# Kernel optimization log

Hardware: AMD Instinct MI355X
Metric: run time of the kernel (lower is better)

## Reference

```python
import jax, jax.numpy as jnp
import numpy as np

EMBED_DIM = 256
NUM_HEADS = 8
MLP_HIDDEN = 1024
EPS = 1e-5
ROPE_BASE = 10000.0
NEG_INF = -1e9


def _ln(x, g, b):
    m = jnp.mean(x, axis=-1, keepdims=True)
    v = jnp.mean((x - m) ** 2, axis=-1, keepdims=True)
    return (x - m) / jnp.sqrt(v + EPS) * g + b


def _proj_qkv(x, W, b):
    # x: (B, L, E); W: (3E, E)
    qkv = x @ W.T + b
    q, k, v = jnp.split(qkv, 3, axis=-1)
    B, L, E = x.shape
    def h(t):
        return t.reshape(B, L, NUM_HEADS, E // NUM_HEADS).transpose(0, 2, 1, 3)
    return h(q), h(k), h(v)


def _rope(x, offset):
    # x: (B, H, L, hd), interleaved even/odd rotation
    hd = x.shape[-1]
    L = x.shape[-2]
    inv_freq = 1.0 / (ROPE_BASE ** (jnp.arange(0, hd, 2, dtype=jnp.float32) / hd))
    t = jnp.arange(L, dtype=jnp.float32) + offset
    freqs = t[:, None] * inv_freq[None, :]  # (L, hd/2)
    cos = jnp.cos(freqs)[None, None].astype(x.dtype)
    sin = jnp.sin(freqs)[None, None].astype(x.dtype)
    xe = x[..., 0::2]
    xo = x[..., 1::2]
    xr = jnp.stack((xe * cos - xo * sin, xe * sin + xo * cos), axis=-1)
    return xr.reshape(x.shape)


def _sdpa(q, k, v, bias):
    scale = 1.0 / jnp.sqrt(jnp.asarray(q.shape[-1], q.dtype))
    s = jnp.einsum('bhqd,bhkd->bhqk', q, k) * scale + bias
    p = jax.nn.softmax(s, axis=-1)
    return jnp.einsum('bhqk,bhkd->bhqd', p, v)


def _mha_self(x, in_w, in_b, out_w, out_b):
    q, k, v = _proj_qkv(x, in_w, in_b)
    o = _sdpa(q, k, v, jnp.zeros((), x.dtype))
    B, H, L, hd = o.shape
    o = o.transpose(0, 2, 1, 3).reshape(B, L, H * hd)
    return o @ out_w.T + out_b


def setup_inputs() -> dict:
    key = jax.random.key(0)
    ks = jax.random.split(key, 20)
    E, Hm = EMBED_DIM, MLP_HIDDEN
    sc = 0.02
    inp = {
        'src': jax.random.normal(ks[0], (8, 128, 64, E), dtype=jnp.float32),
        'src_mask': jax.random.randint(ks[1], (8, 128), 0, 2, dtype=jnp.int32),
        'ctx_qry_split_index': 96,
        'y_in_w': jax.random.normal(ks[2], (3 * E, E)) * sc,
        'y_in_b': jnp.zeros((3 * E,)),
        'y_out_w': jax.random.normal(ks[3], (E, E)) * sc,
        'y_out_b': jnp.zeros((E,)),
        'x_in_w': jax.random.normal(ks[4], (3 * E, E)) * sc,
        'x_in_b': jnp.zeros((3 * E,)),
        'x_out_w': jax.random.normal(ks[5], (E, E)) * sc,
        'x_out_b': jnp.zeros((E,)),
        'w1': jax.random.normal(ks[6], (Hm, E)) * sc,
        'b1': jnp.zeros((Hm,)),
        'w2': jax.random.normal(ks[7], (E, Hm)) * sc,
        'b2': jnp.zeros((E,)),
        'n1_g': jnp.ones((E,)), 'n1_b': jnp.zeros((E,)),
        'n2_g': jnp.ones((E,)), 'n2_b': jnp.zeros((E,)),
        'n3_g': jnp.ones((E,)), 'n3_b': jnp.zeros((E,)),
    }
    return inp


def reference(src, src_mask, ctx_qry_split_index,
              y_in_w, y_in_b, y_out_w, y_out_b,
              x_in_w, x_in_b, x_out_w, x_out_b,
              w1, b1, w2, b2,
              n1_g, n1_b, n2_g, n2_b, n3_g, n3_b):
    bs, R, C, E = src.shape
    S = int(ctx_qry_split_index)
    # ---- y (column-axis) self-attention ----
    x = src.reshape(bs * R, C, E)
    x = jnp.nan_to_num(x, nan=0.0, posinf=0.0, neginf=0.0)
    x = _mha_self(x, y_in_w, y_in_b, y_out_w, y_out_b) + x
    x = x.reshape(bs, R, C, E)
    x = _ln(x, n1_g, n1_b)
    # ---- x (row-axis) attention with ctx/qry split ----
    x = x.transpose(0, 2, 1, 3).reshape(bs * C, R, E)
    x = jnp.nan_to_num(x, nan=0.0, posinf=0.0, neginf=0.0)
    mask_x = jnp.broadcast_to((src_mask > 0)[:, None, :], (bs, C, R)).reshape(bs * C, R)
    kpm_ctx = ~mask_x[:, :S]  # (B, S) True = padded
    bias = jnp.where(kpm_ctx[:, None, None, :], jnp.asarray(NEG_INF, x.dtype), 0.0)
    src_ctx = x[:, :S, :]
    src_qry = x[:, S:, :]
    # ctx self-attention
    q_c, k_c, v_c = _proj_qkv(src_ctx, x_in_w, x_in_b)
    q_c = _rope(q_c, 0)
    k_c = _rope(k_c, 0)
    out_ctx = _sdpa(q_c, k_c, v_c, bias)
    B = bs * C
    out_ctx = out_ctx.transpose(0, 2, 1, 3).reshape(B, S, E)
    out_ctx = out_ctx @ x_out_w.T + x_out_b
    src_ctx = out_ctx + src_ctx
    # qry cross-attention into (updated) ctx
    q_q, _, _ = _proj_qkv(src_qry, x_in_w, x_in_b)
    _, k_c2, v_c2 = _proj_qkv(src_ctx, x_in_w, x_in_b)
    q_q = _rope(q_q, S)
    k_c2 = _rope(k_c2, 0)
    out_qry = _sdpa(q_q, k_c2, v_c2, bias)
    L_qry = R - S
    out_qry = out_qry.transpose(0, 2, 1, 3).reshape(B, L_qry, E)
    out_qry = out_qry @ x_out_w.T + x_out_b
    src_qry = out_qry + src_qry
    x = jnp.concatenate([src_ctx, src_qry], axis=1)
    x = x.reshape(bs, C, R, E).transpose(0, 2, 1, 3)
    x = _ln(x, n2_g, n2_b)
    # ---- FFN ----
    mlp = (jax.nn.gelu(x @ w1.T + b1, approximate=False)) @ w2.T + b2
    x = x + mlp
    return _ln(x, n3_g, n3_b)
```

## Files before the change

### kernel.cpp

```cpp
#include <hip/hip_runtime.h>
#include <hip/hip_bf16.h>
#include <math.h>


#define EDIM 256
#define HD   32
#define SCTX 96

typedef __bf16 bf16x8 __attribute__((ext_vector_type(8)));
typedef float  f32x4  __attribute__((ext_vector_type(4)));
union Frag { bf16x8 v; unsigned short u[8]; };

static __device__ __forceinline__ float b2f(unsigned short u) {
    return __uint_as_float(((unsigned int)u) << 16);
}
static __device__ __forceinline__ unsigned short f2b(float f) {
    unsigned int u = __float_as_uint(f);
    u += 0x7fffu + ((u >> 16) & 1u);
    return (unsigned short)(u >> 16);
}

static __device__ __forceinline__ void gload16(const unsigned short* g, unsigned short* l) {
    __builtin_amdgcn_global_load_lds(
        (const __attribute__((address_space(1))) unsigned int*)g,
        (__attribute__((address_space(3))) unsigned int*)l,
        16, 0, 0);
}

__global__ void detect_kernel(const unsigned int* __restrict__ n1g_raw,
                              int* __restrict__ flag) {
    *flag = (*n1g_raw == 0x3F800000u) ? 1 : 0;
}

struct PtrTable { const void* p[18]; };

__global__ void cvt_kernel(PtrTable t, const int* __restrict__ flag,
                           unsigned short* __restrict__ wp) {
    const int seg_off[19] = {0, 196608, 197376, 262912, 263168, 459776, 460544,
                             526080, 526336, 788480, 789504, 1051648, 1051904,
                             1052160, 1052416, 1052672, 1052928, 1053184, 1053440};
    const int f = *flag;
    int idx = blockIdx.x * blockDim.x + threadIdx.x;
    int stride = gridDim.x * blockDim.x;
    for (int i = idx; i < 1053440; i += stride) {
        int s = 0;
        while (i >= seg_off[s + 1]) ++s;
        int j = i - seg_off[s];
        unsigned short o;
        if (f) o = f2b(((const float*)t.p[s])[j]);
        else   o = ((const unsigned short*)t.p[s])[j];
        wp[i] = o;
    }
}

__global__ void prep_kernel(const void* __restrict__ src,
                            unsigned short* __restrict__ dst,
                            const int* __restrict__ flag, int n4) {
    const int f = *flag;
    int idx = blockIdx.x * blockDim.x + threadIdx.x;
    int stride = gridDim.x * blockDim.x;
    if (f) {
        const float4* s4 = (const float4*)src;
        for (int i = idx; i < n4; i += stride) {
            float4 v = s4[i];
            ushort4 o;
            o.x = ((__float_as_uint(v.x) & 0x7F800000u) == 0x7F800000u) ? 0 : f2b(v.x);
            o.y = ((__float_as_uint(v.y) & 0x7F800000u) == 0x7F800000u) ? 0 : f2b(v.y);
            o.z = ((__float_as_uint(v.z) & 0x7F800000u) == 0x7F800000u) ? 0 : f2b(v.z);
            o.w = ((__float_as_uint(v.w) & 0x7F800000u) == 0x7F800000u) ? 0 : f2b(v.w);
            ((ushort4*)dst)[i] = o;
        }
    } else {
        const ushort4* s4 = (const ushort4*)src;
        for (int i = idx; i < n4; i += stride) {
            ushort4 v = s4[i];
            if ((v.x & 0x7F80u) == 0x7F80u) v.x = 0;
            if ((v.y & 0x7F80u) == 0x7F80u) v.y = 0;
            if ((v.z & 0x7F80u) == 0x7F80u) v.z = 0;
            if ((v.w & 0x7F80u) == 0x7F80u) v.w = 0;
            ((ushort4*)dst)[i] = v;
        }
    }
}

__global__ __launch_bounds__(256) void gemm_mfma(
        const unsigned short* __restrict__ A, int lda,
        const unsigned short* __restrict__ W, int ldw,
        const unsigned short* __restrict__ bias,
        const unsigned short* __restrict__ res,
        unsigned short* __restrict__ out, int ldo,
        int K, int fuse, int pred, const int* __restrict__ splitp) {
    __shared__ __align__(16) unsigned short SH[16384];
    unsigned short* Asb  = SH;
    unsigned short* Bsb  = SH + 8192;
    unsigned short* Slab = SH;

    const int tid = threadIdx.x;

    const int nT   = gridDim.y;
    const int nwg  = gridDim.x * nT;
    const int flat = blockIdx.y * gridDim.x + blockIdx.x;
    const int cpx  = nwg >> 3;
    const int wgid = (flat & 7) * cpx + (flat >> 3);
    const int m0 = (wgid / nT) * 128;
    const int n0 = (wgid % nT) * 128;

    const int wave = tid >> 6;
    const int lane = tid & 63;
    const int wm = (wave >> 1) << 6;
    const int wn = (wave & 1) << 6;
    const int lm = lane & 15;
    const int lq = lane >> 4;

    const int rt = tid >> 3;
    const int ct = (tid & 7) * 8;
    const unsigned short* Ag = A + (size_t)(m0 + rt) * lda + ct;
    const unsigned short* Wg = W + (size_t)(n0 + rt) * ldw + ct;
    const size_t a32 = (size_t)32 * lda, w32 = (size_t)32 * ldw;
    unsigned short* Adst = Asb + wave * 512;
    unsigned short* Bdst = Bsb + wave * 512;

    f32x4 acc[4][4] = {};
    for (int k0 = 0; k0 < K; k0 += 64) {
        __syncthreads();
#pragma unroll
        for (int j = 0; j < 4; ++j) {
            gload16(Ag + j * a32 + k0, Adst + j * 2048);
            gload16(Wg + j * w32 + k0, Bdst + j * 2048);
        }
        __syncthreads();
#pragma unroll
        for (int kk = 0; kk < 2; ++kk) {
            const int ko = kk * 32 + lq * 8;
            bf16x8 af[4], bq[4];
#pragma unroll
            for (int i = 0; i < 4; ++i)
                af[i] = *(const bf16x8*)&Asb[(wm + i * 16 + lm) * 64 + ko];
#pragma unroll
            for (int j = 0; j < 4; ++j)
                bq[j] = *(const bf16x8*)&Bsb[(wn + j * 16 + lm) * 64 + ko];
#pragma unroll
            for (int i = 0; i < 4; ++i)
#pragma unroll
                for (int j = 0; j < 4; ++j)
                    acc[i][j] = __builtin_amdgcn_mfma_f32_16x16x32_bf16(af[i], bq[j], acc[i][j], 0, 0, 0);
        }
    }
    __syncthreads();

    const int S = (pred != 0) ? *splitp : 0;
    float bv[4];
#pragma unroll
    for (int j = 0; j < 4; ++j)
        bv[j] = bias ? b2f(bias[n0 + wn + j * 16 + lm]) : 0.f;

    const int srow = (wave >> 1) * 16 + lq * 4;
    const int sr2 = tid >> 3;
    const int cc = (tid & 7) * 16;
    const int mH = (sr2 >> 4) * 64 + (sr2 & 15);

#pragma unroll
    for (int i = 0; i < 4; ++i) {
#pragma unroll
        for (int j = 0; j < 4; ++j)
#pragma unroll
            for (int r = 0; r < 4; ++r) {
                float x = acc[i][j][r] + bv[j];
                if (fuse == 1) x = 0.5f * x * (1.0f + erff(x * 0.70710678118654752f));
                Slab[(srow + r) * 136 + wn + j * 16 + lm] = f2b(x);
            }
        __syncthreads();
        {
            const int m = m0 + mH + i * 16;
            const int rr = m & 127;
            bool st = true;
            if (pred == 1 && rr >= S) st = false;
            if (pred == 2 && rr < S) st = false;
            if (st) {
#pragma unroll
                for (int h = 0; h < 2; ++h) {
                    uint4 v = *(const uint4*)&Slab[sr2 * 136 + cc + h * 8];
                    if (res) {
                        uint4 rv = *(const uint4*)(res + (size_t)m * 256 + n0 + cc + h * 8);
                        unsigned short* pv = (unsigned short*)&v;
                        const unsigned short* pr = (const unsigned short*)&rv;
#pragma unroll
                        for (int e = 0; e < 8; ++e)
                            pv[e] = f2b(b2f(pv[e]) + b2f(pr[e]));
                    }
                    *(uint4*)(out + (size_t)m * ldo + n0 + cc + h * 8) = v;
                }
            }
        }
        __syncthreads();
    }
}

static __device__ __forceinline__ void rope8(float* t, int p0, float pos) {
#pragma unroll
    for (int p = 0; p < 4; ++p) {
        float invf = exp2f((float)(p0 + p) * -0.8304820237193385f);
        float ang = pos * invf;
        float c = __cosf(ang), s = __sinf(ang);
        float xe = t[2 * p], xo = t[2 * p + 1];
        t[2 * p]     = xe * c - xo * s;
        t[2 * p + 1] = xe * s + xo * c;
    }
}

template<int NQT, int NKT, bool ROPE, bool BIAS>
__global__ __launch_bounds__(64) void attn_mfma(unsigned short* __restrict__ QKV,
                                                const int* __restrict__ mask,
                                                int seqlen, int qoff) {
    constexpr int NK = NKT * 16;
    constexpr int KS = NK / 32;
    const int s = blockIdx.x;
    const int h = blockIdx.y;
    const int lane = threadIdx.x;
    const int lm = lane & 15;
    const int lq = lane >> 4;
    const size_t rowbase = (size_t)s * seqlen;
    const float scale = 0.17677669529663689f;

    __shared__ __align__(16) unsigned short Vs[NK][40];
    __shared__ __align__(16) unsigned short Pt[16][104];
    __shared__ float bias_s[NK];

#pragma unroll
    for (int r0 = 0; r0 < NK; r0 += 16) {
        int r = r0 + (lane >> 2);
        int c = (lane & 3) * 8;
        uint4 v = *(const uint4*)(QKV + (rowbase + r) * 768 + 512 + h * 32 + c);
        *(uint4*)&Vs[r][c] = v;
    }
    if (BIAS) {
        const int b = s >> 6;
        for (int r = lane; r < NK; r += 64)
            bias_s[r] = (mask[b * 128 + r] > 0) ? 0.f : -1e9f;
    }
    Frag kf[NKT];
#pragma unroll
    for (int nt = 0; nt < NKT; ++nt) {
        const int krow = nt * 16 + lm;
        const unsigned short* kp = QKV + (rowbase + krow) * 768 + 256 + h * 32 + lq * 8;
        float t[8];
#pragma unroll
        for (int j = 0; j < 8; ++j) t[j] = b2f(kp[j]);
        if (ROPE) rope8(t, lq * 4, (float)krow);
#pragma unroll
        for (int j = 0; j < 8; ++j) kf[nt].u[j] = f2b(t[j]);
    }
    __syncthreads();
    Frag bvf[KS][2];
#pragma unroll
    for (int ks = 0; ks < KS; ++ks)
#pragma unroll
        for (int dt = 0; dt < 2; ++dt)
#pragma unroll
            for (int j = 0; j < 8; ++j)
                bvf[ks][dt].u[j] = Vs[ks * 32 + lq * 8 + j][dt * 16 + lm];

    for (int mt = 0; mt < NQT; ++mt) {
        Frag qf;
        const int qrow = qoff + mt * 16 + lm;
        {
            const unsigned short* qp = QKV + (rowbase + qrow) * 768 + h * 32 + lq * 8;
            float t[8];
#pragma unroll
            for (int j = 0; j < 8; ++j) t[j] = b2f(qp[j]);
            if (ROPE) rope8(t, lq * 4, (float)qrow);
#pragma unroll
            for (int j = 0; j < 8; ++j) qf.u[j] = f2b(t[j]);
        }
        f32x4 sacc[NKT] = {};
#pragma unroll
        for (int nt = 0; nt < NKT; ++nt)
            sacc[nt] = __builtin_amdgcn_mfma_f32_16x16x32_bf16(qf.v, kf[nt].v, sacc[nt], 0, 0, 0);
        float pv[NKT][4], mx[4], sm[4], inv[4];
#pragma unroll
        for (int r = 0; r < 4; ++r) mx[r] = -3.0e38f;
#pragma unroll
        for (int nt = 0; nt < NKT; ++nt)
#pragma unroll
            for (int r = 0; r < 4; ++r) {
                float x = sacc[nt][r] * scale;
                if (BIAS) x += bias_s[nt * 16 + lm];
                pv[nt][r] = x;
                mx[r] = fmaxf(mx[r], x);
            }
#pragma unroll
        for (int m = 1; m < 16; m <<= 1)
#pragma unroll
            for (int r = 0; r < 4; ++r) mx[r] = fmaxf(mx[r], __shfl_xor(mx[r], m, 64));
#pragma unroll
        for (int r = 0; r < 4; ++r) sm[r] = 0.f;
#pragma unroll
        for (int nt = 0; nt < NKT; ++nt)
#pragma unroll
            for (int r = 0; r < 4; ++r) {
                float p = __expf(pv[nt][r] - mx[r]);
                pv[nt][r] = p;
                sm[r] += p;
            }
#pragma unroll
        for (int m = 1; m < 16; m <<= 1)
#pragma unroll
            for (int r = 0; r < 4; ++r) sm[r] += __shfl_xor(sm[r], m, 64);
#pragma unroll
        for (int r = 0; r < 4; ++r) inv[r] = 1.f / sm[r];
#pragma unroll
        for (int nt = 0; nt < NKT; ++nt)
#pragma unroll
            for (int r = 0; r < 4; ++r)
                Pt[lq * 4 + r][nt * 16 + lm] = f2b(pv[nt][r] * inv[r]);
        __syncthreads();
        f32x4 oacc[2] = {};
#pragma unroll
        for (int ks = 0; ks < KS; ++ks) {
            Frag af;
            af.v = *(const bf16x8*)&Pt[lm][ks * 32 + lq * 8];
#pragma unroll
            for (int dt = 0; dt < 2; ++dt)
                oacc[dt] = __builtin_amdgcn_mfma_f32_16x16x32_bf16(af.v, bvf[ks][dt].v, oacc[dt], 0, 0, 0);
        }
#pragma unroll
        for (int dt = 0; dt < 2; ++dt)
#pragma unroll
            for (int r = 0; r < 4; ++r) {
                const int m = qoff + mt * 16 + lq * 4 + r;
                QKV[(rowbase + m) * 768 + h * 32 + dt * 16 + lm] = f2b(oacc[dt][r]);
            }
        __syncthreads();
    }
}

__global__ __launch_bounds__(64) void ln_permute_kernel(
        const unsigned short* __restrict__ X,
        const unsigned short* __restrict__ gam,
        const unsigned short* __restrict__ bet,
        void* __restrict__ Y, int mode, const int* __restrict__ flag) {
    const int t = blockIdx.x;
    const int tid = threadIdx.x;
    const int e = tid << 2;
    ushort4 xv = *(const ushort4*)(X + (size_t)t * EDIM + e);
    float v0 = b2f(xv.x), v1 = b2f(xv.y), v2 = b2f(xv.z), v3 = b2f(xv.w);
    float s = v0 + v1 + v2 + v3;
#pragma unroll
    for (int m = 32; m > 0; m >>= 1) s += __shfl_xor(s, m, 64);
    float mean = s * (1.f / EDIM);
    float d0 = v0 - mean, d1 = v1 - mean, d2 = v2 - mean, d3 = v3 - mean;
    float q = d0 * d0 + d1 * d1 + d2 * d2 + d3 * d3;
#pragma unroll
    for (int m = 32; m > 0; m >>= 1) q += __shfl_xor(q, m, 64);
    float rstd = rsqrtf(q * (1.f / EDIM) + 1e-5f);
    float g0 = b2f(gam[e]), g1 = b2f(gam[e + 1]), g2 = b2f(gam[e + 2]), g3 = b2f(gam[e + 3]);
    float b0 = b2f(bet[e]), b1 = b2f(bet[e + 1]), b2_ = b2f(bet[e + 2]), b3 = b2f(bet[e + 3]);
    float y0 = d0 * rstd * g0 + b0;
    float y1 = d1 * rstd * g1 + b1;
    float y2 = d2 * rstd * g2 + b2_;
    float y3 = d3 * rstd * g3 + b3;
    size_t drow;
    if (mode == 0) {
        int b = t >> 13, r = (t >> 6) & 127, c = t & 63;
        drow = ((size_t)b << 13) + ((size_t)c << 7) + (size_t)r;
    } else if (mode == 1) {
        int b = t >> 13, c = (t >> 7) & 63, r = t & 127;
        drow = ((size_t)b << 13) + ((size_t)r << 6) + (size_t)c;
    } else {
        drow = (size_t)t;
    }
    if (mode == 2 && *flag) {
        float4 o4 = make_float4(y0, y1, y2, y3);
        *(float4*)((float*)Y + drow * EDIM + e) = o4;
    } else {
        ushort4 o;
        o.x = f2b(y0); o.y = f2b(y1); o.z = f2b(y2); o.w = f2b(y3);
        *(ushort4*)((unsigned short*)Y + drow * EDIM + e) = o;
    }
}

extern "C" void kernel_launch(void* const* d_in, const int* in_sizes, int n_in,
                              void* d_out, int out_size, void* d_ws, size_t ws_size,
                              hipStream_t stream) {
    (void)in_sizes; (void)n_in; (void)out_size; (void)ws_size;
    const void* src  = d_in[0];
    const int*  mask = (const int*)d_in[1];
    const int*  split= (const int*)d_in[2];

    int*            flag = (int*)d_ws;
    unsigned short* wp   = (unsigned short*)((char*)d_ws + 1024);
    unsigned short* Xa   = (unsigned short*)((char*)d_ws + (size_t)4 * 1024 * 1024);
    unsigned short* Xb   = Xa + (size_t)16777216;
    unsigned short* QKV  = Xb + (size_t)16777216;
    unsigned short* HID  = QKV;

    const unsigned short* y_in_w  = wp + 0;
    const unsigned short* y_in_b  = wp + 196608;
    const unsigned short* y_out_w = wp + 197376;
    const unsigned short* y_out_b = wp + 262912;
    const unsigned short* x_in_w  = wp + 263168;
    const unsigned short* x_in_b  = wp + 459776;
    const unsigned short* x_out_w = wp + 460544;
    const unsigned short* x_out_b = wp + 526080;
    const unsigned short* w1      = wp + 526336;
    const unsigned short* b1      = wp + 788480;
    const unsigned short* w2      = wp + 789504;
    const unsigned short* b2      = wp + 1051648;
    const unsigned short* n1_g    = wp + 1051904;
    const unsigned short* n1_b    = wp + 1052160;
    const unsigned short* n2_g    = wp + 1052416;
    const unsigned short* n2_b    = wp + 1052672;
    const unsigned short* n3_g    = wp + 1052928;
    const unsigned short* n3_b    = wp + 1053184;

    detect_kernel<<<1, 1, 0, stream>>>((const unsigned int*)d_in[15], flag);

    PtrTable pt;
    for (int i = 0; i < 18; ++i) pt.p[i] = d_in[3 + i];
    cvt_kernel<<<512, 256, 0, stream>>>(pt, flag, wp);

    prep_kernel<<<4096, 256, 0, stream>>>(src, Xa, flag, 4194304);
    gemm_mfma<<<dim3(512, 6), 256, 0, stream>>>(Xa, 256, y_in_w, 256, y_in_b, nullptr, QKV, 768, 256, 0, 0, nullptr);
    attn_mfma<4, 4, false, false><<<dim3(1024, 8), 64, 0, stream>>>(QKV, mask, 64, 0);
    gemm_mfma<<<dim3(512, 2), 256, 0, stream>>>(QKV, 768, y_out_w, 256, y_out_b, Xa, Xa, 256, 256, 0, 0, nullptr);
    ln_permute_kernel<<<65536, 64, 0, stream>>>(Xa, n1_g, n1_b, Xb, 0, flag);
    gemm_mfma<<<dim3(512, 6), 256, 0, stream>>>(Xb, 256, x_in_w, 256, x_in_b, nullptr, QKV, 768, 256, 0, 0, nullptr);
    attn_mfma<6, 6, true, true><<<dim3(512, 8), 64, 0, stream>>>(QKV, mask, 128, 0);
    gemm_mfma<<<dim3(512, 2), 256, 0, stream>>>(QKV, 768, x_out_w, 256, x_out_b, Xb, Xb, 256, 256, 0, 1, split);
    gemm_mfma<<<dim3(512, 4), 256, 0, stream>>>(Xb, 256, x_in_w + 65536, 256, x_in_b + 256, nullptr, QKV + 256, 768, 256, 0, 0, nullptr);
    attn_mfma<2, 6, true, true><<<dim3(512, 8), 64, 0, stream>>>(QKV, mask, 128, 96);
    gemm_mfma<<<dim3(512, 2), 256, 0, stream>>>(QKV, 768, x_out_w, 256, x_out_b, Xb, Xb, 256, 256, 0, 2, split);
    ln_permute_kernel<<<65536, 64, 0, stream>>>(Xb, n2_g, n2_b, Xa, 1, flag);
    gemm_mfma<<<dim3(512, 4), 256, 0, stream>>>(Xa, 256, w1, 256, b1, nullptr, HID, 512, 256, 1, 0, nullptr);
    gemm_mfma<<<dim3(512, 2), 256, 0, stream>>>(HID, 512, w2, 1024, b2, Xa, Xb, 256, 512, 0, 0, nullptr);
    gemm_mfma<<<dim3(512, 4), 256, 0, stream>>>(Xa, 256, w1 + 512 * 256, 256, b1 + 512, nullptr, HID, 512, 256, 1, 0, nullptr);
    gemm_mfma<<<dim3(512, 2), 256, 0, stream>>>(HID, 512, w2 + 512, 1024, nullptr, Xb, Xb, 256, 512, 0, 0, nullptr);
    ln_permute_kernel<<<65536, 64, 0, stream>>>(Xb, n3_g, n3_b, d_out, 2, flag);
}
```

Baseline: 746.3 us.

## Double-buffer GEMM LDS tiles to overlap global loads with MFMA

Doubles the shared-memory buffer in the MFMA GEMM kernel so the next K-tile is fetched into LDS via global_load_lds while the current tile is being multiplied. This also drops one barrier per K step. The aim is to hide global memory latency behind compute. In exchange, LDS use rises to 64KB per block, which may reduce occupancy. Correctness now relies on a single barrier per iteration covering both the async load completion and the buffer reuse.

```diff
diff --git a/kernel.cpp b/kernel.cpp
--- a/kernel.cpp
+++ b/kernel.cpp
@@ -90,9 +90,7 @@
         const unsigned short* __restrict__ res,
         unsigned short* __restrict__ out, int ldo,
         int K, int fuse, int pred, const int* __restrict__ splitp) {
-    __shared__ __align__(16) unsigned short SH[16384];
-    unsigned short* Asb  = SH;
-    unsigned short* Bsb  = SH + 8192;
+    __shared__ __align__(16) unsigned short SH[32768];
     unsigned short* Slab = SH;
 
     const int tid = threadIdx.x;
@@ -117,36 +115,50 @@
     const unsigned short* Ag = A + (size_t)(m0 + rt) * lda + ct;
     const unsigned short* Wg = W + (size_t)(n0 + rt) * ldw + ct;
     const size_t a32 = (size_t)32 * lda, w32 = (size_t)32 * ldw;
-    unsigned short* Adst = Asb + wave * 512;
-    unsigned short* Bdst = Bsb + wave * 512;
+    const int wofs = wave * 512;
 
     f32x4 acc[4][4] = {};
-    for (int k0 = 0; k0 < K; k0 += 64) {
-        __syncthreads();
-#pragma unroll
-        for (int j = 0; j < 4; ++j) {
-            gload16(Ag + j * a32 + k0, Adst + j * 2048);
-            gload16(Wg + j * w32 + k0, Bdst + j * 2048);
-        }
-        __syncthreads();
+    const int nk = K >> 6;
+
+#pragma unroll
+    for (int j = 0; j < 4; ++j) {
+        gload16(Ag + j * a32, SH + wofs + j * 2048);
+        gload16(Wg + j * w32, SH + 8192 + wofs + j * 2048);
+    }
+    __syncthreads();
+
+    int cur = 0;
+    for (int t = 0; t < nk; ++t) {
+        if (t + 1 < nk) {
+            const int kn = (t + 1) << 6;
+            unsigned short* Ad = SH + ((cur ^ 1) << 14) + wofs;
+#pragma unroll
+            for (int j = 0; j < 4; ++j) {
+                gload16(Ag + j * a32 + kn, Ad + j * 2048);
+                gload16(Wg + j * w32 + kn, Ad + 8192 + j * 2048);
+            }
+        }
+        const unsigned short* As = SH + (cur << 14);
+        const unsigned short* Bs = As + 8192;
 #pragma unroll
         for (int kk = 0; kk < 2; ++kk) {
             const int ko = kk * 32 + lq * 8;
             bf16x8 af[4], bq[4];
 #pragma unroll
             for (int i = 0; i < 4; ++i)
-                af[i] = *(const bf16x8*)&Asb[(wm + i * 16 + lm) * 64 + ko];
+                af[i] = *(const bf16x8*)&As[(wm + i * 16 + lm) * 64 + ko];
 #pragma unroll
             for (int j = 0; j < 4; ++j)
-                bq[j] = *(const bf16x8*)&Bsb[(wn + j * 16 + lm) * 64 + ko];
+                bq[j] = *(const bf16x8*)&Bs[(wn + j * 16 + lm) * 64 + ko];
 #pragma unroll
             for (int i = 0; i < 4; ++i)
 #pragma unroll
                 for (int j = 0; j < 4; ++j)
                     acc[i][j] = __builtin_amdgcn_mfma_f32_16x16x32_bf16(af[i], bq[j], acc[i][j], 0, 0, 0);
         }
-    }
-    __syncthreads();
+        __syncthreads();
+        cur ^= 1;
+    }
 
     const int S = (pred != 0) ? *splitp : 0;
     float bv[4];
```

After: 725.2 us. 2.8% less time.

## Load GEMM fragments directly from global into registers with double buffering

Applied to the files above, without the earlier changes.

Replaces the LDS-staged tile loads (global_load_lds plus two barriers per k-step) in the MFMA GEMM with direct per-lane global loads of bf16x8 fragments into registers. Two register sets are ping-ponged so the next k-slice loads while the current one issues MFMAs. This removes LDS traffic and the block-wide syncs, but every wave now fetches its own A/B rows with no sharing across waves. That doubles global/L2 traffic and uses 16-byte strided accesses that coalesce less well. The shared buffer shrinks to only the epilogue slab, which may allow higher occupancy.

```diff
diff --git a/kernel.cpp b/kernel.cpp
--- a/kernel.cpp
+++ b/kernel.cpp
@@ -18,13 +18,6 @@
     unsigned int u = __float_as_uint(f);
     u += 0x7fffu + ((u >> 16) & 1u);
     return (unsigned short)(u >> 16);
-}
-
-static __device__ __forceinline__ void gload16(const unsigned short* g, unsigned short* l) {
-    __builtin_amdgcn_global_load_lds(
-        (const __attribute__((address_space(1))) unsigned int*)g,
-        (__attribute__((address_space(3))) unsigned int*)l,
-        16, 0, 0);
 }
 
 __global__ void detect_kernel(const unsigned int* __restrict__ n1g_raw,
@@ -83,6 +76,26 @@
     }
 }
 
+#define LOADF(af, bf, kk)                                                     \
+    {                                                                         \
+        _Pragma("unroll")                                                     \
+        for (int i_ = 0; i_ < 4; ++i_)                                        \
+            af[i_] = *(const bf16x8*)(Ab + i_ * a16 + (kk));                  \
+        _Pragma("unroll")                                                     \
+        for (int j_ = 0; j_ < 4; ++j_)                                        \
+            bf[j_] = *(const bf16x8*)(Bb + j_ * b16 + (kk));                  \
+    }
+
+#define MMF(af, bf)                                                           \
+    {                                                                         \
+        _Pragma("unroll")                                                     \
+        for (int i_ = 0; i_ < 4; ++i_)                                        \
+            _Pragma("unroll")                                                 \
+            for (int j_ = 0; j_ < 4; ++j_)                                    \
+                acc[i_][j_] = __builtin_amdgcn_mfma_f32_16x16x32_bf16(        \
+                    af[i_], bf[j_], acc[i_][j_], 0, 0, 0);                    \
+    }
+
 __global__ __launch_bounds__(256) void gemm_mfma(
         const unsigned short* __restrict__ A, int lda,
         const unsigned short* __restrict__ W, int ldw,
@@ -90,10 +103,7 @@
         const unsigned short* __restrict__ res,
         unsigned short* __restrict__ out, int ldo,
         int K, int fuse, int pred, const int* __restrict__ splitp) {
-    __shared__ __align__(16) unsigned short SH[16384];
-    unsigned short* Asb  = SH;
-    unsigned short* Bsb  = SH + 8192;
-    unsigned short* Slab = SH;
+    __shared__ __align__(16) unsigned short Slab[32 * 136];
 
     const int tid = threadIdx.x;
 
@@ -112,41 +122,21 @@
     const int lm = lane & 15;
     const int lq = lane >> 4;
 
-    const int rt = tid >> 3;
-    const int ct = (tid & 7) * 8;
-    const unsigned short* Ag = A + (size_t)(m0 + rt) * lda + ct;
-    const unsigned short* Wg = W + (size_t)(n0 + rt) * ldw + ct;
-    const size_t a32 = (size_t)32 * lda, w32 = (size_t)32 * ldw;
-    unsigned short* Adst = Asb + wave * 512;
-    unsigned short* Bdst = Bsb + wave * 512;
+    const unsigned short* Ab = A + (size_t)(m0 + wm + lm) * lda + lq * 8;
+    const unsigned short* Bb = W + (size_t)(n0 + wn + lm) * ldw + lq * 8;
+    const size_t a16 = (size_t)16 * lda, b16 = (size_t)16 * ldw;
 
     f32x4 acc[4][4] = {};
-    for (int k0 = 0; k0 < K; k0 += 64) {
-        __syncthreads();
-#pragma unroll
-        for (int j = 0; j < 4; ++j) {
-            gload16(Ag + j * a32 + k0, Adst + j * 2048);
-            gload16(Wg + j * w32 + k0, Bdst + j * 2048);
-        }
-        __syncthreads();
-#pragma unroll
-        for (int kk = 0; kk < 2; ++kk) {
-            const int ko = kk * 32 + lq * 8;
-            bf16x8 af[4], bq[4];
-#pragma unroll
-            for (int i = 0; i < 4; ++i)
-                af[i] = *(const bf16x8*)&Asb[(wm + i * 16 + lm) * 64 + ko];
-#pragma unroll
-            for (int j = 0; j < 4; ++j)
-                bq[j] = *(const bf16x8*)&Bsb[(wn + j * 16 + lm) * 64 + ko];
-#pragma unroll
-            for (int i = 0; i < 4; ++i)
-#pragma unroll
-                for (int j = 0; j < 4; ++j)
-                    acc[i][j] = __builtin_amdgcn_mfma_f32_16x16x32_bf16(af[i], bq[j], acc[i][j], 0, 0, 0);
-        }
-    }
-    __syncthreads();
+    const int nk = K >> 5;
+
+    bf16x8 a0[4], b0[4], a1[4], b1[4];
+    LOADF(a0, b0, 0);
+    for (int t = 0; t < nk; t += 2) {
+        LOADF(a1, b1, (t + 1) << 5);
+        MMF(a0, b0);
+        if (t + 2 < nk) LOADF(a0, b0, (t + 2) << 5);
+        MMF(a1, b1);
+    }
 
     const int S = (pred != 0) ? *splitp : 0;
     float bv[4];
```

After: 1.044 ms. 1.4x slower.
